# Kernel optimization log

Measured on AMD Instinct MI355X. Metric: run time of the kernel, lower is better.

## Reference

```python
import jax, jax.numpy as jnp
import numpy as np

NEG_INF = np.float32(-np.inf)

def setup_inputs() -> dict:
    key = jax.random.key(0)
    k1, k2 = jax.random.split(key)
    x = jax.random.normal(k1, (8, 4, 512, 512), dtype=jnp.float32)
    weight = jax.random.normal(k2, (8, 4, 5, 5), dtype=jnp.float32)
    return {"x": x, "weight": weight}

def reference(x, weight):
    # Morphological (max-plus) dilation:
    # out[n,co,h,w] = max_{ci,kh,kw} x[n,ci,h+kh-oh, w+kw-ow] + weight[co,ci,kh,kw]
    # origin (oh,ow) = kernel_size // 2; out-of-bounds -> padding_value (-inf).
    N, Ci, H, W = x.shape
    Co, _, Kh, Kw = weight.shape
    oh, ow = Kh // 2, Kw // 2
    xp = jnp.pad(x, ((0, 0), (0, 0), (oh, Kh - 1 - oh), (ow, Kw - 1 - ow)),
                 constant_values=NEG_INF)
    out = jnp.full((N, Co, H, W), NEG_INF, dtype=x.dtype)
    # small fixed loop over the Kh*Kw structuring-element taps; data dims vectorized
    for kh in range(Kh):
        for kw in range(Kw):
            win = xp[:, :, kh:kh + H, kw:kw + W]            # [N,Ci,H,W]
            w_tap = weight[:, :, kh, kw]                     # [Co,Ci]
            cand = jnp.max(win[:, None] + w_tap[None, :, :, None, None], axis=2)  # [N,Co,H,W]
            out = jnp.maximum(out, cand)
    return out
```

## Files before the change

### kernel.cpp

```cpp
#include <hip/hip_runtime.h>
#include <hip/hip_bf16.h>

#define NEG_INF (-__builtin_inff())

__global__ __launch_bounds__(256) void dil2d_kernel(const float* __restrict__ x,
                                                    const float* __restrict__ w,
                                                    float* __restrict__ out) {
    const int Ci = 4, Co = 8, H = 512, W = 512;

    const int tid = threadIdx.x;
    const int wg  = tid & 127;
    const int w0  = wg << 2;
    const int rib = tid >> 7;
    const int b   = blockIdx.x;
    const int n   = b >> 8;
    const int h   = ((b & 255) << 1) + rib;

    float acc[Co][4];
#pragma unroll
    for (int co = 0; co < Co; ++co)
#pragma unroll
        for (int j = 0; j < 4; ++j) acc[co][j] = NEG_INF;

    const float* xn = x + n * (Ci * H * W);

    for (int ci = 0; ci < Ci; ++ci) {
        const float* xc = xn + ci * (H * W);
        const float* wc = w + ci * 25;
        for (int kh = 0; kh < 5; ++kh) {
            const int r = h + kh - 2;
            if (r < 0 || r >= H) continue;
            const float* xr = xc + r * W;

            float xv[8];
            {
                const int off_lo = (w0 == 0)   ? 0   : (w0 - 2);
                const int off_hi = (w0 == 508) ? 508 : (w0 + 4);
                const float2 lo  = *(const float2*)(xr + off_lo);
                const float4 mid = *(const float4*)(xr + w0);
                const float2 hi  = *(const float2*)(xr + off_hi);
                xv[0] = (w0 == 0)   ? NEG_INF : lo.x;
                xv[1] = (w0 == 0)   ? NEG_INF : lo.y;
                xv[2] = mid.x; xv[3] = mid.y; xv[4] = mid.z; xv[5] = mid.w;
                xv[6] = (w0 == 508) ? NEG_INF : hi.x;
                xv[7] = (w0 == 508) ? NEG_INF : hi.y;
            }

            const float* wk = wc + kh * 5;
#pragma unroll
            for (int co = 0; co < Co; ++co) {
                const float* wco = wk + co * (Ci * 25);
                const float wv0 = wco[0], wv1 = wco[1], wv2 = wco[2],
                            wv3 = wco[3], wv4 = wco[4];
#pragma unroll
                for (int j = 0; j < 4; ++j) {
                    float m  = acc[co][j];
                    float t0 = xv[j]     + wv0;
                    float t1 = xv[j + 1] + wv1;
                    m = fmaxf(m, fmaxf(t0, t1));
                    float t2 = xv[j + 2] + wv2;
                    float t3 = xv[j + 3] + wv3;
                    m = fmaxf(m, fmaxf(t2, t3));
                    m = fmaxf(m, xv[j + 4] + wv4);
                    acc[co][j] = m;
                }
            }
        }
    }

    float* on = out + n * (Co * H * W) + h * W + w0;
#pragma unroll
    for (int co = 0; co < Co; ++co) {
        float4 v = make_float4(acc[co][0], acc[co][1], acc[co][2], acc[co][3]);
        *(float4*)(on + co * (H * W)) = v;
    }
}

extern "C" void kernel_launch(void* const* d_in, const int* in_sizes, int n_in,
                              void* d_out, int out_size, void* d_ws, size_t ws_size,
                              hipStream_t stream) {
    const float* x = (const float*)d_in[0];
    const float* w = (const float*)d_in[1];
    float* out     = (float*)d_out;

    dim3 grid(2048), block(256);
    hipLaunchKernelGGL(dil2d_kernel, grid, block, 0, stream, x, w, out);
}
```

Baseline: 139.8 us.

## Use packed f32 adds over output-channel pairs with LDS weights and wider tiles

Weights are staged in shared memory, interleaved so that pairs of output channels sit next to each other and can be loaded as two-float vectors. Each add of an input value to two channels' weights is done with one v_pk_add_f32, which roughly halves the add instruction count. Each thread now computes 8 output columns instead of 4 and each block covers 4 rows, which halves the grid and lowers halo-load overhead per output. The costs are more accumulator registers, capped by launch_bounds(256,2), and a block barrier for the weight staging.

```diff
diff --git a/kernel.cpp b/kernel.cpp
--- a/kernel.cpp
+++ b/kernel.cpp
@@ -1,78 +1,119 @@
 #include <hip/hip_runtime.h>
-#include <hip/hip_bf16.h>
 
 #define NEG_INF (-__builtin_inff())
 
-__global__ __launch_bounds__(256) void dil2d_kernel(const float* __restrict__ x,
-                                                    const float* __restrict__ w,
-                                                    float* __restrict__ out) {
-    const int Ci = 4, Co = 8, H = 512, W = 512;
+typedef float v2f __attribute__((ext_vector_type(2)));
+
+static __device__ __forceinline__ v2f pk_add(v2f a, v2f b) {
+    v2f d;
+    asm("v_pk_add_f32 %0, %1, %2" : "=v"(d) : "v"(a), "v"(b));
+    return d;
+}
+
+__global__ __launch_bounds__(256, 2) void dil2d_kernel(const float* __restrict__ x,
+                                                       const float* __restrict__ w,
+                                                       float* __restrict__ out) {
+    const int Ci = 4, H = 512, W = 512;
+
+    __shared__ float wl[800];
+    {
+        int i = threadIdx.x;
+#pragma unroll
+        for (int rep = 0; rep < 4; ++rep, i += 256) {
+            if (i < 800) {
+                const int co = i & 7;
+                const int t  = i >> 3;
+                const int kw = t % 5;
+                const int kh = (t / 5) % 5;
+                const int ci = t / 25;
+                wl[i] = w[((co * 4 + ci) * 5 + kh) * 5 + kw];
+            }
+        }
+    }
+    __syncthreads();
 
     const int tid = threadIdx.x;
-    const int wg  = tid & 127;
-    const int w0  = wg << 2;
-    const int rib = tid >> 7;
+    const int wg  = tid & 63;
+    const int w0  = wg << 3;
+    const int rib = tid >> 6;
     const int b   = blockIdx.x;
-    const int n   = b >> 8;
-    const int h   = ((b & 255) << 1) + rib;
+    const int n   = b >> 7;
+    const int h   = ((b & 127) << 2) + rib;
 
-    float acc[Co][4];
+    float accx[4][8], accy[4][8];
 #pragma unroll
-    for (int co = 0; co < Co; ++co)
+    for (int p = 0; p < 4; ++p)
 #pragma unroll
-        for (int j = 0; j < 4; ++j) acc[co][j] = NEG_INF;
+        for (int j = 0; j < 8; ++j) { accx[p][j] = NEG_INF; accy[p][j] = NEG_INF; }
 
     const float* xn = x + n * (Ci * H * W);
 
     for (int ci = 0; ci < Ci; ++ci) {
         const float* xc = xn + ci * (H * W);
-        const float* wc = w + ci * 25;
+        const v2f*   wc = (const v2f*)(wl + ci * 200);
         for (int kh = 0; kh < 5; ++kh) {
             const int r = h + kh - 2;
             if (r < 0 || r >= H) continue;
             const float* xr = xc + r * W;
 
-            float xv[8];
-            {
-                const int off_lo = (w0 == 0)   ? 0   : (w0 - 2);
-                const int off_hi = (w0 == 508) ? 508 : (w0 + 4);
-                const float2 lo  = *(const float2*)(xr + off_lo);
-                const float4 mid = *(const float4*)(xr + w0);
-                const float2 hi  = *(const float2*)(xr + off_hi);
-                xv[0] = (w0 == 0)   ? NEG_INF : lo.x;
-                xv[1] = (w0 == 0)   ? NEG_INF : lo.y;
-                xv[2] = mid.x; xv[3] = mid.y; xv[4] = mid.z; xv[5] = mid.w;
-                xv[6] = (w0 == 508) ? NEG_INF : hi.x;
-                xv[7] = (w0 == 508) ? NEG_INF : hi.y;
-            }
+            const int off_lo = (w0 == 0)   ? 0   : (w0 - 4);
+            const int off_hi = (w0 == 504) ? 504 : (w0 + 8);
+            const float4 lo4 = *(const float4*)(xr + off_lo);
+            const float4 m0  = *(const float4*)(xr + w0);
+            const float4 m1  = *(const float4*)(xr + w0 + 4);
+            const float4 hi4 = *(const float4*)(xr + off_hi);
 
-            const float* wk = wc + kh * 5;
+            float xv[12];
+            xv[0]  = (w0 == 0)   ? NEG_INF : lo4.z;
+            xv[1]  = (w0 == 0)   ? NEG_INF : lo4.w;
+            xv[2]  = m0.x; xv[3] = m0.y; xv[4] = m0.z; xv[5] = m0.w;
+            xv[6]  = m1.x; xv[7] = m1.y; xv[8] = m1.z; xv[9] = m1.w;
+            xv[10] = (w0 == 504) ? NEG_INF : hi4.x;
+            xv[11] = (w0 == 504) ? NEG_INF : hi4.y;
+
+            v2f xb[12];
 #pragma unroll
-            for (int co = 0; co < Co; ++co) {
-                const float* wco = wk + co * (Ci * 25);
-                const float wv0 = wco[0], wv1 = wco[1], wv2 = wco[2],
-                            wv3 = wco[3], wv4 = wco[4];
+            for (int m = 0; m < 12; ++m) { v2f t; t.x = xv[m]; t.y = xv[m]; xb[m] = t; }
+
+            const v2f* wk = wc + kh * 20;
 #pragma unroll
-                for (int j = 0; j < 4; ++j) {
-                    float m  = acc[co][j];
-                    float t0 = xv[j]     + wv0;
-                    float t1 = xv[j + 1] + wv1;
-                    m = fmaxf(m, fmaxf(t0, t1));
-                    float t2 = xv[j + 2] + wv2;
-                    float t3 = xv[j + 3] + wv3;
-                    m = fmaxf(m, fmaxf(t2, t3));
-                    m = fmaxf(m, xv[j + 4] + wv4);
-                    acc[co][j] = m;
+            for (int p = 0; p < 4; ++p) {
+                v2f w2[5];
+#pragma unroll
+                for (int k = 0; k < 5; ++k) w2[k] = wk[k * 4 + p];
+#pragma unroll
+                for (int j = 0; j < 8; ++j) {
+                    const v2f t0 = pk_add(xb[j],     w2[0]);
+                    const v2f t1 = pk_add(xb[j + 1], w2[1]);
+                    const v2f t2 = pk_add(xb[j + 2], w2[2]);
+                    const v2f t3 = pk_add(xb[j + 3], w2[3]);
+                    const v2f t4 = pk_add(xb[j + 4], w2[4]);
+                    float ax = accx[p][j], ay = accy[p][j];
+                    ax = fmaxf(ax, fmaxf(t0.x, t1.x));
+                    ay = fmaxf(ay, fmaxf(t0.y, t1.y));
+                    ax = fmaxf(ax, fmaxf(t2.x, t3.x));
+                    ay = fmaxf(ay, fmaxf(t2.y, t3.y));
+                    ax = fmaxf(ax, t4.x);
+                    ay = fmaxf(ay, t4.y);
+                    accx[p][j] = ax; accy[p][j] = ay;
                 }
             }
         }
     }
 
-    float* on = out + n * (Co * H * W) + h * W + w0;
+    float* on = out + n * (8 * H * W) + h * W + w0;
 #pragma unroll
-    for (int co = 0; co < Co; ++co) {
-        float4 v = make_float4(acc[co][0], acc[co][1], acc[co][2], acc[co][3]);
-        *(float4*)(on + co * (H * W)) = v;
+    for (int p = 0; p < 4; ++p) {
+        const float4 a0 = make_float4(accx[p][0], accx[p][1], accx[p][2], accx[p][3]);
+        const float4 a1 = make_float4(accx[p][4], accx[p][5], accx[p][6], accx[p][7]);
+        const float4 b0 = make_float4(accy[p][0], accy[p][1], accy[p][2], accy[p][3]);
+        const float4 b1 = make_float4(accy[p][4], accy[p][5], accy[p][6], accy[p][7]);
+        float* o0 = on + (2 * p) * (H * W);
+        float* o1 = o0 + (H * W);
+        *(float4*)(o0)     = a0;
+        *(float4*)(o0 + 4) = a1;
+        *(float4*)(o1)     = b0;
+        *(float4*)(o1 + 4) = b1;
     }
 }
 
@@ -83,6 +124,6 @@
     const float* w = (const float*)d_in[1];
     float* out     = (float*)d_out;
 
-    dim3 grid(2048), block(256);
+    dim3 grid(1024), block(256);
     hipLaunchKernelGGL(dil2d_kernel, grid, block, 0, stream, x, w, out);
 }
```

Result: slower. 163.2 us (+16.7%).

## Split output channels across wavefronts and widen per-thread column tile to 8

Applied to the files above, without the earlier changes.

Each thread now computes 8 adjacent columns for 4 output channels instead of 4 columns for all 8 channels. The two wavefront halves split the channel range, and the channel offset is made wave-uniform with readfirstlane so weight loads can be scalar. The per-thread halo is a smaller fraction of the loaded row, but each input row is now loaded by two wavefronts. Launch bounds also request 4 blocks per CU.

```diff
diff --git a/kernel.cpp b/kernel.cpp
--- a/kernel.cpp
+++ b/kernel.cpp
@@ -1,60 +1,65 @@
 #include <hip/hip_runtime.h>
-#include <hip/hip_bf16.h>
 
 #define NEG_INF (-__builtin_inff())
 
-__global__ __launch_bounds__(256) void dil2d_kernel(const float* __restrict__ x,
-                                                    const float* __restrict__ w,
-                                                    float* __restrict__ out) {
-    const int Ci = 4, Co = 8, H = 512, W = 512;
+__global__ __launch_bounds__(256, 4) void dil2d_kernel(const float* __restrict__ x,
+                                                       const float* __restrict__ w,
+                                                       float* __restrict__ out) {
+    const int Ci = 4, H = 512, W = 512;
 
     const int tid = threadIdx.x;
-    const int wg  = tid & 127;
-    const int w0  = wg << 2;
+    const int wg  = tid & 63;
+    const int w0  = wg << 3;
+    const int coh = (tid >> 6) & 1;
     const int rib = tid >> 7;
+    const int co0 = __builtin_amdgcn_readfirstlane(coh << 2);
     const int b   = blockIdx.x;
     const int n   = b >> 8;
     const int h   = ((b & 255) << 1) + rib;
 
-    float acc[Co][4];
+    float acc[4][8];
 #pragma unroll
-    for (int co = 0; co < Co; ++co)
+    for (int cs = 0; cs < 4; ++cs)
 #pragma unroll
-        for (int j = 0; j < 4; ++j) acc[co][j] = NEG_INF;
+        for (int j = 0; j < 8; ++j) acc[cs][j] = NEG_INF;
 
     const float* xn = x + n * (Ci * H * W);
 
+    const bool lo_edge = (w0 == 0);
+    const bool hi_edge = (w0 == 504);
+    const int  off_lo  = lo_edge ? 0   : (w0 - 4);
+    const int  off_hi  = hi_edge ? 504 : (w0 + 8);
+
     for (int ci = 0; ci < Ci; ++ci) {
-        const float* xc = xn + ci * (H * W);
-        const float* wc = w + ci * 25;
+        const float* xc  = xn + ci * (H * W);
+        const float* wci = w + co0 * (Ci * 25) + ci * 25;
         for (int kh = 0; kh < 5; ++kh) {
             const int r = h + kh - 2;
             if (r < 0 || r >= H) continue;
             const float* xr = xc + r * W;
 
-            float xv[8];
-            {
-                const int off_lo = (w0 == 0)   ? 0   : (w0 - 2);
-                const int off_hi = (w0 == 508) ? 508 : (w0 + 4);
-                const float2 lo  = *(const float2*)(xr + off_lo);
-                const float4 mid = *(const float4*)(xr + w0);
-                const float2 hi  = *(const float2*)(xr + off_hi);
-                xv[0] = (w0 == 0)   ? NEG_INF : lo.x;
-                xv[1] = (w0 == 0)   ? NEG_INF : lo.y;
-                xv[2] = mid.x; xv[3] = mid.y; xv[4] = mid.z; xv[5] = mid.w;
-                xv[6] = (w0 == 508) ? NEG_INF : hi.x;
-                xv[7] = (w0 == 508) ? NEG_INF : hi.y;
-            }
+            const float4 lo4 = *(const float4*)(xr + off_lo);
+            const float4 m0  = *(const float4*)(xr + w0);
+            const float4 m1  = *(const float4*)(xr + w0 + 4);
+            const float4 hi4 = *(const float4*)(xr + off_hi);
 
-            const float* wk = wc + kh * 5;
+            float xv[12];
+            xv[0]  = lo_edge ? NEG_INF : lo4.z;
+            xv[1]  = lo_edge ? NEG_INF : lo4.w;
+            xv[2]  = m0.x; xv[3] = m0.y; xv[4] = m0.z; xv[5] = m0.w;
+            xv[6]  = m1.x; xv[7] = m1.y; xv[8] = m1.z; xv[9] = m1.w;
+            xv[10] = hi_edge ? NEG_INF : hi4.x;
+            xv[11] = hi_edge ? NEG_INF : hi4.y;
+
+            const float* wk = wci + kh * 5;
 #pragma unroll
-            for (int co = 0; co < Co; ++co) {
-                const float* wco = wk + co * (Ci * 25);
+            for (int cs = 0; cs < 4; ++cs) {
+                const float* wco = wk + cs * (Ci * 25);
                 const float wv0 = wco[0], wv1 = wco[1], wv2 = wco[2],
                             wv3 = wco[3], wv4 = wco[4];
 #pragma unroll
-                for (int j = 0; j < 4; ++j) {
-                    float m  = acc[co][j];
+                for (int j = 0; j < 8; ++j) {
+                    float m  = acc[cs][j];
                     float t0 = xv[j]     + wv0;
                     float t1 = xv[j + 1] + wv1;
                     m = fmaxf(m, fmaxf(t0, t1));
@@ -62,17 +67,18 @@
                     float t3 = xv[j + 3] + wv3;
                     m = fmaxf(m, fmaxf(t2, t3));
                     m = fmaxf(m, xv[j + 4] + wv4);
-                    acc[co][j] = m;
+                    acc[cs][j] = m;
                 }
             }
         }
     }
 
-    float* on = out + n * (Co * H * W) + h * W + w0;
+    float* on = out + n * (8 * H * W) + (co0) * (H * W) + h * W + w0;
 #pragma unroll
-    for (int co = 0; co < Co; ++co) {
-        float4 v = make_float4(acc[co][0], acc[co][1], acc[co][2], acc[co][3]);
-        *(float4*)(on + co * (H * W)) = v;
+    for (int cs = 0; cs < 4; ++cs) {
+        float* o = on + cs * (H * W);
+        *(float4*)(o)     = make_float4(acc[cs][0], acc[cs][1], acc[cs][2], acc[cs][3]);
+        *(float4*)(o + 4) = make_float4(acc[cs][4], acc[cs][5], acc[cs][6], acc[cs][7]);
     }
 }
 
```

Result: no change. 138.6 us (-0.9%).
